# Optimization experiments

Hardware: AMD Instinct MI355X
Metric: run time of the kernel (lower is better)

The kernel has to match this reference:

```python
import jax, jax.numpy as jnp
import numpy as np

KDIM = 8192
EPS = 1e-8  # F.cosine_similarity default eps


def _encoder(x, W1, b1, W2, b2, W3, b3):
    # x: [..., KDIM] -> [..., 128]; Linear(KDIM,512)->ReLU->Linear(512,256)->ReLU->Linear(256,128)
    h = jax.nn.relu(x @ W1 + b1)
    h = jax.nn.relu(h @ W2 + b2)
    return h @ W3 + b3


def setup_inputs() -> dict:
    key = jax.random.key(0)
    ks = jax.random.split(key, 16)

    def lin(k, fan_in, fan_out):
        bound = 1.0 / np.sqrt(fan_in)
        kw, kb = jax.random.split(k)
        W = jax.random.uniform(kw, (fan_in, fan_out), jnp.float32, -bound, bound)
        b = jax.random.uniform(kb, (fan_out,), jnp.float32, -bound, bound)
        return W, b

    W1, b1 = lin(ks[0], KDIM, 512)
    W2, b2 = lin(ks[1], 512, 256)
    W3, b3 = lin(ks[2], 256, 128)
    Wi1, bi1 = lin(ks[3], 128 + 6, 64)
    Wi2, bi2 = lin(ks[4], 64, 32)
    Wi3, bi3 = lin(ks[5], 32, 1)

    return {
        "new_knowledge": jax.random.normal(ks[6], (KDIM,), jnp.float32),
        "existing_knowledge": jax.random.normal(ks[7], (10, KDIM), jnp.float32),
        "math_metrics": jax.random.uniform(ks[8], (6,), jnp.float32),
        "W1": W1, "b1": b1, "W2": W2, "b2": b2, "W3": W3, "b3": b3,
        "Wi1": Wi1, "bi1": bi1, "Wi2": Wi2, "bi2": bi2, "Wi3": Wi3, "bi3": bi3,
    }


def reference(new_knowledge, existing_knowledge, math_metrics,
              W1, b1, W2, b2, W3, b3, Wi1, bi1, Wi2, bi2, Wi3, bi3):
    # Encode new knowledge: [128]
    new_enc = _encoder(new_knowledge, W1, b1, W2, b2, W3, b3)
    # Batched encode of the (up to 10) existing knowledge vectors: [10, 128]
    ex_enc = _encoder(existing_knowledge, W1, b1, W2, b2, W3, b3)

    # Per-item geometric distance (L2 norm of difference)
    diff = new_enc[None, :] - ex_enc                     # [10, 128]
    geo_dist = jnp.sqrt(jnp.sum(diff * diff, axis=-1))   # [10]

    # Per-item cosine similarity with torch eps clamping
    new_n = jnp.maximum(jnp.linalg.norm(new_enc), EPS)
    ex_n = jnp.maximum(jnp.linalg.norm(ex_enc, axis=-1), EPS)  # [10]
    cos = (ex_enc @ new_enc) / (new_n * ex_n)            # [10]

    avg_consistency = jnp.mean(geo_dist - cos)

    # Mathematical-constraint integrator MLP on [128 + 6]
    combined = jnp.concatenate([new_enc, math_metrics])  # [134]
    h = jax.nn.relu(combined @ Wi1 + bi1)
    h = jax.nn.relu(h @ Wi2 + bi2)
    quality = h @ Wi3 + bi3                              # [1]

    integration_loss = jnp.exp(-quality)                 # [1]
    total = jnp.squeeze(avg_consistency + integration_loss)
    return total
```

## Files before the change

### kernel.cpp

```cpp
#include <hip/hip_runtime.h>
#include <math.h>

#define EPS 1e-8f
typedef float f32x4 __attribute__((ext_vector_type(4)));

__device__ __forceinline__ float wredsum(float v) {
#pragma unroll
  for (int o = 32; o > 0; o >>= 1) v += __shfl_down(v, o, 64);
  return v;
}

__device__ __forceinline__ void fma8(const float4* w, const float4 a,
                                     const float4 b, float4& c) {
  const float xs[8] = {a.x, a.y, a.z, a.w, b.x, b.y, b.z, b.w};
#pragma unroll
  for (int i = 0; i < 8; ++i) {
    c.x = fmaf(xs[i], w[i].x, c.x);
    c.y = fmaf(xs[i], w[i].y, c.y);
    c.z = fmaf(xs[i], w[i].z, c.z);
    c.w = fmaf(xs[i], w[i].w, c.w);
  }
}

__global__ __launch_bounds__(256, 2) void k_l1(const float* __restrict__ xn,
                                               const float* __restrict__ xe,
                                               const float* __restrict__ W1,
                                               float* __restrict__ p1,
                                               int* __restrict__ bars) {
  if (blockIdx.x == 0 && blockIdx.y == 0 && threadIdx.x == 0) {
    bars[0] = 0; bars[1] = 0;
  }
  __shared__ float red[11 * 32 * 36];
  const int cg  = threadIdx.x & 7;
  const int ks  = threadIdx.x >> 3;
  const int col = blockIdx.x * 32 + cg * 4;
  const int k0  = blockIdx.y * 256 + ks * 8;

  float4 w[8];
#pragma unroll
  for (int i = 0; i < 8; ++i)
    w[i] = *(const float4*)&W1[(size_t)(k0 + i) * 512 + col];

  float4 acc[11];
#pragma unroll
  for (int r = 0; r < 11; ++r) acc[r] = make_float4(0.f, 0.f, 0.f, 0.f);

  {
    const float4 a = *(const float4*)&xn[k0];
    const float4 b = *(const float4*)&xn[k0 + 4];
    fma8(w, a, b, acc[0]);
  }
#pragma unroll
  for (int r = 0; r < 10; ++r) {
    const float4 a = *(const float4*)&xe[r * 8192 + k0];
    const float4 b = *(const float4*)&xe[r * 8192 + k0 + 4];
    fma8(w, a, b, acc[r + 1]);
  }

#pragma unroll
  for (int r = 0; r < 11; ++r)
    *(float4*)&red[(r * 32 + ks) * 36 + cg * 4] = acc[r];
  __syncthreads();

  for (int o = threadIdx.x; o < 352; o += 256) {
    const int r = o >> 5, c = o & 31;
    float s = 0.f;
#pragma unroll
    for (int k = 0; k < 32; ++k) s += red[(r * 32 + k) * 36 + c];
    p1[((size_t)blockIdx.y * 11 + r) * 512 + blockIdx.x * 32 + c] = s;
  }
}

__global__ __launch_bounds__(1024) void k_tail(
    const float* __restrict__ p1, const float* __restrict__ b1,
    const float* __restrict__ W2, const float* __restrict__ b2,
    const float* __restrict__ W3, const float* __restrict__ b3,
    const float* __restrict__ mm,
    const float* __restrict__ Wi1, const float* __restrict__ bi1,
    const float* __restrict__ Wi2, const float* __restrict__ bi2,
    const float* __restrict__ Wi3, const float* __restrict__ bi3,
    float* __restrict__ p2, float* __restrict__ encp,
    int* __restrict__ bars, float* __restrict__ out) {
  __shared__ __align__(16) float smem[12368];
  __shared__ int tick;
  const int t = threadIdx.x;
  const int j = blockIdx.x;

  const int c = t & 255, kg = t >> 8;
  float w2r[8];
#pragma unroll
  for (int kk = 0; kk < 8; ++kk)
    w2r[kk] = W2[(size_t)(j * 32 + kg * 8 + kk) * 256 + c];

  float* h1s = smem;
  if (t < 352) {
    const int r = t >> 5, cc = t & 31;
    const int col = j * 32 + cc;
    float s = b1[col];
#pragma unroll
    for (int ch = 0; ch < 32; ++ch) s += p1[(size_t)(ch * 11 + r) * 512 + col];
    h1s[r * 32 + cc] = fmaxf(s, 0.f);
  }
  __syncthreads();

  float* redA = smem + 1024;
  {
    float acc[11];
#pragma unroll
    for (int r = 0; r < 11; ++r) acc[r] = 0.f;
#pragma unroll
    for (int kk = 0; kk < 8; ++kk) {
      const int kl = kg * 8 + kk;
#pragma unroll
      for (int r = 0; r < 11; ++r)
        acc[r] = fmaf(h1s[r * 32 + kl], w2r[kk], acc[r]);
    }
#pragma unroll
    for (int r = 0; r < 11; ++r) redA[(kg * 11 + r) * 256 + c] = acc[r];
  }
  __syncthreads();
  for (int o = t; o < 2816; o += 1024) {
    const int r = o >> 8, cc = o & 255;
    p2[(size_t)j * 2816 + o] = redA[r * 256 + cc] + redA[(11 + r) * 256 + cc] +
                               redA[(22 + r) * 256 + cc] +
                               redA[(33 + r) * 256 + cc];
  }

  __syncthreads();
  if (t == 0) {
    __threadfence();
    tick = __hip_atomic_fetch_add(&bars[0], 1, __ATOMIC_ACQ_REL,
                                  __HIP_MEMORY_SCOPE_AGENT);
  }
  __syncthreads();
  const int rank = tick;
  if (rank < 12) return;
  const int q = rank - 12;

  const int c3 = t & 127, kg3 = t >> 7;
  float w3r[8];
#pragma unroll
  for (int kk = 0; kk < 8; ++kk)
    w3r[kk] = W3[(size_t)(q * 64 + kg3 * 8 + kk) * 128 + c3];

  if (t == 0) {
    while (__hip_atomic_load(&bars[0], __ATOMIC_RELAXED,
                             __HIP_MEMORY_SCOPE_AGENT) < 16)
      __builtin_amdgcn_s_sleep(1);
    __threadfence();
  }
  __syncthreads();

  float* h2q = smem;
  if (t < 704) {
    const int r = t >> 6, kk = t & 63;
    const int col = q * 64 + kk;
    float s = b2[col];
#pragma unroll
    for (int jj = 0; jj < 16; ++jj) s += p2[(size_t)jj * 2816 + r * 256 + col];
    h2q[r * 64 + kk] = fmaxf(s, 0.f);
  }
  __syncthreads();
  float* redB = smem + 1024;
  {
    float acc[11];
#pragma unroll
    for (int r = 0; r < 11; ++r) acc[r] = 0.f;
#pragma unroll
    for (int kk = 0; kk < 8; ++kk) {
      const int kl = kg3 * 8 + kk;
#pragma unroll
      for (int r = 0; r < 11; ++r)
        acc[r] = fmaf(h2q[r * 64 + kl], w3r[kk], acc[r]);
    }
#pragma unroll
    for (int r = 0; r < 11; ++r) redB[(kg3 * 11 + r) * 128 + c3] = acc[r];
  }
  __syncthreads();
  for (int o = t; o < 1408; o += 1024) {
    const int r = o >> 7, cc = o & 127;
    float s = 0.f;
#pragma unroll
    for (int g = 0; g < 8; ++g) s += redB[(g * 11 + r) * 128 + cc];
    encp[(size_t)q * 1408 + o] = s;
  }

  __syncthreads();
  if (t == 0) {
    __threadfence();
    tick = __hip_atomic_fetch_add(&bars[1], 1, __ATOMIC_ACQ_REL,
                                  __HIP_MEMORY_SCOPE_AGENT);
  }
  __syncthreads();
  if (tick != 3) return;
  if (t == 0) __threadfence();
  __syncthreads();

  float* encs = smem;
  float* wi1s = smem + 1536;
  float* wi2s = smem + 10112;
  float* comb = smem + 12160;
  float* h1b  = smem + 12296;
  for (int i = t; i < 2144; i += 1024)
    ((f32x4*)wi1s)[i] = ((const f32x4*)Wi1)[i];
  if (t < 512) ((f32x4*)wi2s)[t] = ((const f32x4*)Wi2)[t];
  for (int o = t; o < 1408; o += 1024) {
    float s = b3[o & 127];
#pragma unroll
    for (int g = 0; g < 4; ++g) s += encp[(size_t)g * 1408 + o];
    encs[o] = s;
  }
  __syncthreads();

  float consist = 0.f;
  float n0 = 0.f, n1 = 0.f;
  if (t < 64) {
    n0 = encs[t]; n1 = encs[64 + t];
    comb[t] = n0; comb[64 + t] = n1;
    if (t < 6) comb[128 + t] = mm[t];
  }
  __syncthreads();
  if (t < 64) {
    const float nn = wredsum(n0 * n0 + n1 * n1);
#pragma unroll
    for (int r = 1; r <= 10; ++r) {
      const float e0 = encs[r * 128 + t];
      const float e1 = encs[r * 128 + 64 + t];
      const float d0 = e0 - n0, d1 = e1 - n1;
      const float g  = wredsum(d0 * d0 + d1 * d1);
      const float qq = wredsum(e0 * e0 + e1 * e1);
      const float dd = wredsum(e0 * n0 + e1 * n1);
      if (t == 0) {
        const float geo = sqrtf(g);
        const float den = fmaxf(sqrtf(nn), EPS) * fmaxf(sqrtf(qq), EPS);
        consist += geo - dd / den;
      }
    }
  } else if (t < 128) {
    const int tt = t - 64;
    float h = bi1[tt];
#pragma unroll 4
    for (int k = 0; k < 134; ++k) h = fmaf(comb[k], wi1s[k * 64 + tt], h);
    h1b[tt] = fmaxf(h, 0.f);
  }
  __syncthreads();
  if (t < 64) {
    float part = 0.f;
    if (t < 32) {
      float hh = bi2[t];
#pragma unroll 8
      for (int k = 0; k < 64; ++k) hh = fmaf(h1b[k], wi2s[k * 32 + t], hh);
      part = fmaxf(hh, 0.f) * Wi3[t];
    }
    const float qual = wredsum(part);
    if (t == 0) out[0] = consist * 0.1f + expf(-(qual + bi3[0]));
  }
}

extern "C" void kernel_launch(void* const* d_in, const int* in_sizes, int n_in,
                              void* d_out, int out_size, void* d_ws, size_t ws_size,
                              hipStream_t stream) {
  (void)in_sizes; (void)n_in; (void)out_size; (void)ws_size;
  const float* xn  = (const float*)d_in[0];
  const float* xe  = (const float*)d_in[1];
  const float* mm  = (const float*)d_in[2];
  const float* W1  = (const float*)d_in[3];
  const float* b1  = (const float*)d_in[4];
  const float* W2  = (const float*)d_in[5];
  const float* b2  = (const float*)d_in[6];
  const float* W3  = (const float*)d_in[7];
  const float* b3  = (const float*)d_in[8];
  const float* Wi1 = (const float*)d_in[9];
  const float* bi1 = (const float*)d_in[10];
  const float* Wi2 = (const float*)d_in[11];
  const float* bi2 = (const float*)d_in[12];
  const float* Wi3 = (const float*)d_in[13];
  const float* bi3 = (const float*)d_in[14];
  float* out = (float*)d_out;

  char* ws = (char*)d_ws;
  float* p1   = (float*)(ws);
  float* p2   = (float*)(ws + 720896);
  float* encp = (float*)(ws + 901120);
  int*   bars = (int*)  (ws + 923648);

  hipLaunchKernelGGL(k_l1,   dim3(16, 32), dim3(256),  0, stream, xn, xe, W1, p1, bars);
  hipLaunchKernelGGL(k_tail, dim3(16),     dim3(1024), 0, stream,
                     p1, b1, W2, b2, W3, b3, mm,
                     Wi1, bi1, Wi2, bi2, Wi3, bi3, p2, encp, bars, out);
}
```

Baseline: 109.4 us.

## Fuse layer-1 and tail kernels into one launch with per-tile flag dependencies

```diff
diff --git a/kernel.cpp b/kernel.cpp
--- a/kernel.cpp
+++ b/kernel.cpp
@@ -2,12 +2,19 @@
 #include <math.h>
 
 #define EPS 1e-8f
+#define MAGIC 0x1F2E3D4C
 typedef float f32x4 __attribute__((ext_vector_type(4)));
 
 __device__ __forceinline__ float wredsum(float v) {
 #pragma unroll
   for (int o = 32; o > 0; o >>= 1) v += __shfl_down(v, o, 64);
   return v;
+}
+
+__device__ __forceinline__ void waitflag(const int* f) {
+  while (__hip_atomic_load(f, __ATOMIC_RELAXED, __HIP_MEMORY_SCOPE_AGENT) !=
+         MAGIC)
+    __builtin_amdgcn_s_sleep(2);
 }
 
 __device__ __forceinline__ void fma8(const float4* w, const float4 a,
@@ -22,79 +29,86 @@
   }
 }
 
-__global__ __launch_bounds__(256, 2) void k_l1(const float* __restrict__ xn,
-                                               const float* __restrict__ xe,
-                                               const float* __restrict__ W1,
-                                               float* __restrict__ p1,
-                                               int* __restrict__ bars) {
-  if (blockIdx.x == 0 && blockIdx.y == 0 && threadIdx.x == 0) {
-    bars[0] = 0; bars[1] = 0;
-  }
-  __shared__ float red[11 * 32 * 36];
-  const int cg  = threadIdx.x & 7;
-  const int ks  = threadIdx.x >> 3;
-  const int col = blockIdx.x * 32 + cg * 4;
-  const int k0  = blockIdx.y * 256 + ks * 8;
-
-  float4 w[8];
-#pragma unroll
-  for (int i = 0; i < 8; ++i)
-    w[i] = *(const float4*)&W1[(size_t)(k0 + i) * 512 + col];
-
-  float4 acc[11];
-#pragma unroll
-  for (int r = 0; r < 11; ++r) acc[r] = make_float4(0.f, 0.f, 0.f, 0.f);
-
-  {
-    const float4 a = *(const float4*)&xn[k0];
-    const float4 b = *(const float4*)&xn[k0 + 4];
-    fma8(w, a, b, acc[0]);
-  }
-#pragma unroll
-  for (int r = 0; r < 10; ++r) {
-    const float4 a = *(const float4*)&xe[r * 8192 + k0];
-    const float4 b = *(const float4*)&xe[r * 8192 + k0 + 4];
-    fma8(w, a, b, acc[r + 1]);
-  }
-
-#pragma unroll
-  for (int r = 0; r < 11; ++r)
-    *(float4*)&red[(r * 32 + ks) * 36 + cg * 4] = acc[r];
-  __syncthreads();
-
-  for (int o = threadIdx.x; o < 352; o += 256) {
-    const int r = o >> 5, c = o & 31;
-    float s = 0.f;
-#pragma unroll
-    for (int k = 0; k < 32; ++k) s += red[(r * 32 + k) * 36 + c];
-    p1[((size_t)blockIdx.y * 11 + r) * 512 + blockIdx.x * 32 + c] = s;
-  }
-}
-
-__global__ __launch_bounds__(1024) void k_tail(
-    const float* __restrict__ p1, const float* __restrict__ b1,
+__global__ __launch_bounds__(256, 2) void k_all(
+    const float* __restrict__ xn, const float* __restrict__ xe,
+    const float* __restrict__ W1, const float* __restrict__ b1,
     const float* __restrict__ W2, const float* __restrict__ b2,
     const float* __restrict__ W3, const float* __restrict__ b3,
     const float* __restrict__ mm,
     const float* __restrict__ Wi1, const float* __restrict__ bi1,
     const float* __restrict__ Wi2, const float* __restrict__ bi2,
     const float* __restrict__ Wi3, const float* __restrict__ bi3,
-    float* __restrict__ p2, float* __restrict__ encp,
-    int* __restrict__ bars, float* __restrict__ out) {
-  __shared__ __align__(16) float smem[12368];
-  __shared__ int tick;
+    float* __restrict__ p1, float* __restrict__ p2, float* __restrict__ encp,
+    int* __restrict__ fA, int* __restrict__ fB, int* __restrict__ fC,
+    float* __restrict__ out) {
+  __shared__ __align__(16) float smem[12672];
   const int t = threadIdx.x;
-  const int j = blockIdx.x;
-
-  const int c = t & 255, kg = t >> 8;
-  float w2r[8];
-#pragma unroll
-  for (int kk = 0; kk < 8; ++kk)
-    w2r[kk] = W2[(size_t)(j * 32 + kg * 8 + kk) * 256 + c];
+  const int b = blockIdx.x;
+
+  if (b < 512) {
+    const int bx = b & 15, by = b >> 4;
+    const int cg = t & 7, ks = t >> 3;
+    const int col = bx * 32 + cg * 4;
+    const int k0  = by * 256 + ks * 8;
+
+    float4 w[8];
+#pragma unroll
+    for (int i = 0; i < 8; ++i)
+      w[i] = *(const float4*)&W1[(size_t)(k0 + i) * 512 + col];
+
+    float4 acc[11];
+#pragma unroll
+    for (int r = 0; r < 11; ++r) acc[r] = make_float4(0.f, 0.f, 0.f, 0.f);
+    {
+      const float4 a = *(const float4*)&xn[k0];
+      const float4 bb = *(const float4*)&xn[k0 + 4];
+      fma8(w, a, bb, acc[0]);
+    }
+#pragma unroll
+    for (int r = 0; r < 10; ++r) {
+      const float4 a = *(const float4*)&xe[r * 8192 + k0];
+      const float4 bb = *(const float4*)&xe[r * 8192 + k0 + 4];
+      fma8(w, a, bb, acc[r + 1]);
+    }
+
+    float* red = smem;
+#pragma unroll
+    for (int r = 0; r < 11; ++r)
+      *(float4*)&red[(r * 32 + ks) * 36 + cg * 4] = acc[r];
+    __syncthreads();
+
+    for (int o = t; o < 352; o += 256) {
+      const int r = o >> 5, c = o & 31;
+      float s = 0.f;
+#pragma unroll
+      for (int k = 0; k < 32; ++k) s += red[(r * 32 + k) * 36 + c];
+      p1[((size_t)by * 11 + r) * 512 + bx * 32 + c] = s;
+    }
+    __syncthreads();
+    if (t == 0) {
+      __threadfence();
+      __hip_atomic_store(&fA[b], MAGIC, __ATOMIC_RELAXED,
+                         __HIP_MEMORY_SCOPE_AGENT);
+    }
+    return;
+  }
+
+  const int j = b - 512;
+  const int c = t;
+
+  float w2r[32];
+#pragma unroll
+  for (int i = 0; i < 32; ++i)
+    w2r[i] = W2[(size_t)(j * 32 + i) * 256 + c];
+
+  if (t < 32) waitflag(&fA[j + 16 * t]);
+  __syncthreads();
+  if (t == 0) __threadfence();
+  __syncthreads();
 
   float* h1s = smem;
-  if (t < 352) {
-    const int r = t >> 5, cc = t & 31;
+  for (int o = t; o < 352; o += 256) {
+    const int r = o >> 5, cc = o & 31;
     const int col = j * 32 + cc;
     float s = b1[col];
 #pragma unroll
@@ -102,9 +116,9 @@
     h1s[r * 32 + cc] = fmaxf(s, 0.f);
   }
   __syncthreads();
-
   float* redA = smem + 1024;
-  {
+#pragma unroll
+  for (int kg = 0; kg < 4; ++kg) {
     float acc[11];
 #pragma unroll
     for (int r = 0; r < 11; ++r) acc[r] = 0.f;
@@ -113,47 +127,53 @@
       const int kl = kg * 8 + kk;
 #pragma unroll
       for (int r = 0; r < 11; ++r)
-        acc[r] = fmaf(h1s[r * 32 + kl], w2r[kk], acc[r]);
+        acc[r] = fmaf(h1s[r * 32 + kl], w2r[kg * 8 + kk], acc[r]);
     }
 #pragma unroll
     for (int r = 0; r < 11; ++r) redA[(kg * 11 + r) * 256 + c] = acc[r];
   }
   __syncthreads();
-  for (int o = t; o < 2816; o += 1024) {
+  for (int o = t; o < 2816; o += 256) {
     const int r = o >> 8, cc = o & 255;
     p2[(size_t)j * 2816 + o] = redA[r * 256 + cc] + redA[(11 + r) * 256 + cc] +
                                redA[(22 + r) * 256 + cc] +
                                redA[(33 + r) * 256 + cc];
   }
-
   __syncthreads();
   if (t == 0) {
     __threadfence();
-    tick = __hip_atomic_fetch_add(&bars[0], 1, __ATOMIC_ACQ_REL,
-                                  __HIP_MEMORY_SCOPE_AGENT);
-  }
-  __syncthreads();
-  const int rank = tick;
-  if (rank < 12) return;
-  const int q = rank - 12;
-
-  const int c3 = t & 127, kg3 = t >> 7;
-  float w3r[8];
-#pragma unroll
-  for (int kk = 0; kk < 8; ++kk)
-    w3r[kk] = W3[(size_t)(q * 64 + kg3 * 8 + kk) * 128 + c3];
-
-  if (t == 0) {
-    while (__hip_atomic_load(&bars[0], __ATOMIC_RELAXED,
-                             __HIP_MEMORY_SCOPE_AGENT) < 16)
-      __builtin_amdgcn_s_sleep(1);
-    __threadfence();
-  }
+    __hip_atomic_store(&fB[j], MAGIC, __ATOMIC_RELAXED,
+                       __HIP_MEMORY_SCOPE_AGENT);
+  }
+
+  if (j < 12) {
+    float dead = 0.f;
+    const int g = j * 256 + t;
+    if (g < 2144)      dead += ((const f32x4*)Wi1)[g][0];
+    else if (g < 2656) dead += ((const f32x4*)Wi2)[g - 2144][0];
+    else if (g < 2672) dead += ((const f32x4*)bi1)[g - 2656][0];
+    else if (g < 2704) dead += ((const f32x4*)b3)[g - 2672][0];
+    else if (g < 2712) dead += ((const f32x4*)bi2)[g - 2704][0];
+    else if (g < 2720) dead += ((const f32x4*)Wi3)[g - 2712][0];
+    asm volatile("" ::"v"(dead));
+    return;
+  }
+  const int q = j - 12;
+
+  const int c3 = t & 127, half = t >> 7;
+  float w3r[32];
+#pragma unroll
+  for (int i = 0; i < 32; ++i)
+    w3r[i] = W3[(size_t)(q * 64 + half * 32 + i) * 128 + c3];
+
+  if (t < 16) waitflag(&fB[t]);
+  __syncthreads();
+  if (t == 0) __threadfence();
   __syncthreads();
 
   float* h2q = smem;
-  if (t < 704) {
-    const int r = t >> 6, kk = t & 63;
+  for (int o = t; o < 704; o += 256) {
+    const int r = o >> 6, kk = o & 63;
     const int col = q * 64 + kk;
     float s = b2[col];
 #pragma unroll
@@ -162,7 +182,9 @@
   }
   __syncthreads();
   float* redB = smem + 1024;
-  {
+#pragma unroll
+  for (int m = 0; m < 4; ++m) {
+    const int kg3 = half * 4 + m;
     float acc[11];
 #pragma unroll
     for (int r = 0; r < 11; ++r) acc[r] = 0.f;
@@ -171,28 +193,29 @@
       const int kl = kg3 * 8 + kk;
 #pragma unroll
       for (int r = 0; r < 11; ++r)
-        acc[r] = fmaf(h2q[r * 64 + kl], w3r[kk], acc[r]);
+        acc[r] = fmaf(h2q[r * 64 + kl], w3r[m * 8 + kk], acc[r]);
     }
 #pragma unroll
     for (int r = 0; r < 11; ++r) redB[(kg3 * 11 + r) * 128 + c3] = acc[r];
   }
   __syncthreads();
-  for (int o = t; o < 1408; o += 1024) {
+  for (int o = t; o < 1408; o += 256) {
     const int r = o >> 7, cc = o & 127;
     float s = 0.f;
 #pragma unroll
     for (int g = 0; g < 8; ++g) s += redB[(g * 11 + r) * 128 + cc];
     encp[(size_t)q * 1408 + o] = s;
   }
-
   __syncthreads();
   if (t == 0) {
     __threadfence();
-    tick = __hip_atomic_fetch_add(&bars[1], 1, __ATOMIC_ACQ_REL,
-                                  __HIP_MEMORY_SCOPE_AGENT);
-  }
-  __syncthreads();
-  if (tick != 3) return;
+    __hip_atomic_store(&fC[q], MAGIC, __ATOMIC_RELAXED,
+                       __HIP_MEMORY_SCOPE_AGENT);
+  }
+  if (j != 15) return;
+
+  if (t < 4) waitflag(&fC[t]);
+  __syncthreads();
   if (t == 0) __threadfence();
   __syncthreads();
 
@@ -201,10 +224,11 @@
   float* wi2s = smem + 10112;
   float* comb = smem + 12160;
   float* h1b  = smem + 12296;
-  for (int i = t; i < 2144; i += 1024)
+  for (int i = t; i < 2144; i += 256)
     ((f32x4*)wi1s)[i] = ((const f32x4*)Wi1)[i];
-  if (t < 512) ((f32x4*)wi2s)[t] = ((const f32x4*)Wi2)[t];
-  for (int o = t; o < 1408; o += 1024) {
+  for (int i = t; i < 512; i += 256)
+    ((f32x4*)wi2s)[i] = ((const f32x4*)Wi2)[i];
+  for (int o = t; o < 1408; o += 256) {
     float s = b3[o & 127];
 #pragma unroll
     for (int g = 0; g < 4; ++g) s += encp[(size_t)g * 1408 + o];
@@ -238,10 +262,10 @@
     }
   } else if (t < 128) {
     const int tt = t - 64;
-    float h = bi1[tt];
+    float hh = bi1[tt];
 #pragma unroll 4
-    for (int k = 0; k < 134; ++k) h = fmaf(comb[k], wi1s[k * 64 + tt], h);
-    h1b[tt] = fmaxf(h, 0.f);
+    for (int k = 0; k < 134; ++k) hh = fmaf(comb[k], wi1s[k * 64 + tt], hh);
+    h1b[tt] = fmaxf(hh, 0.f);
   }
   __syncthreads();
   if (t < 64) {
@@ -255,6 +279,14 @@
     const float qual = wredsum(part);
     if (t == 0) out[0] = consist * 0.1f + expf(-(qual + bi3[0]));
   }
+
+  __syncthreads();
+  for (int i = t; i < 512; i += 256)
+    __hip_atomic_store(&fA[i], 0, __ATOMIC_RELAXED, __HIP_MEMORY_SCOPE_AGENT);
+  if (t < 16)
+    __hip_atomic_store(&fB[t], 0, __ATOMIC_RELAXED, __HIP_MEMORY_SCOPE_AGENT);
+  if (t < 4)
+    __hip_atomic_store(&fC[t], 0, __ATOMIC_RELAXED, __HIP_MEMORY_SCOPE_AGENT);
 }
 
 extern "C" void kernel_launch(void* const* d_in, const int* in_sizes, int n_in,
@@ -282,10 +314,12 @@
   float* p1   = (float*)(ws);
   float* p2   = (float*)(ws + 720896);
   float* encp = (float*)(ws + 901120);
-  int*   bars = (int*)  (ws + 923648);
-
-  hipLaunchKernelGGL(k_l1,   dim3(16, 32), dim3(256),  0, stream, xn, xe, W1, p1, bars);
-  hipLaunchKernelGGL(k_tail, dim3(16),     dim3(1024), 0, stream,
-                     p1, b1, W2, b2, W3, b3, mm,
-                     Wi1, bi1, Wi2, bi2, Wi3, bi3, p2, encp, bars, out);
-}
+  int*   fA   = (int*)  (ws + 923648);
+  int*   fB   = (int*)  (ws + 925696);
+  int*   fC   = (int*)  (ws + 925760);
+
+  hipLaunchKernelGGL(k_all, dim3(528), dim3(256), 0, stream,
+                     xn, xe, W1, b1, W2, b2, W3, b3, mm,
+                     Wi1, bi1, Wi2, bi2, Wi3, bi3,
+                     p1, p2, encp, fA, fB, fC, out);
+}
```

Measured after the change: 127.7 us. 1.17x slower.

## Split tail kernel into role-specialized blocks with per-block ready flags

Applied to the files above, without the earlier changes.

```diff
diff --git a/kernel.cpp b/kernel.cpp
--- a/kernel.cpp
+++ b/kernel.cpp
@@ -2,12 +2,19 @@
 #include <math.h>
 
 #define EPS 1e-8f
+#define MAGIC 0x1F2E3D4C
 typedef float f32x4 __attribute__((ext_vector_type(4)));
 
 __device__ __forceinline__ float wredsum(float v) {
 #pragma unroll
   for (int o = 32; o > 0; o >>= 1) v += __shfl_down(v, o, 64);
   return v;
+}
+
+__device__ __forceinline__ void waitflag(const int* f) {
+  while (__hip_atomic_load(f, __ATOMIC_RELAXED, __HIP_MEMORY_SCOPE_AGENT) !=
+         MAGIC)
+    __builtin_amdgcn_s_sleep(2);
 }
 
 __device__ __forceinline__ void fma8(const float4* w, const float4 a,
@@ -26,10 +33,9 @@
                                                const float* __restrict__ xe,
                                                const float* __restrict__ W1,
                                                float* __restrict__ p1,
-                                               int* __restrict__ bars) {
-  if (blockIdx.x == 0 && blockIdx.y == 0 && threadIdx.x == 0) {
-    bars[0] = 0; bars[1] = 0;
-  }
+                                               int* __restrict__ flg) {
+  if (blockIdx.x == 0 && blockIdx.y == 0 && threadIdx.x < 40)
+    flg[threadIdx.x] = 0;
   __shared__ float red[11 * 32 * 36];
   const int cg  = threadIdx.x & 7;
   const int ks  = threadIdx.x >> 3;
@@ -44,7 +50,6 @@
   float4 acc[11];
 #pragma unroll
   for (int r = 0; r < 11; ++r) acc[r] = make_float4(0.f, 0.f, 0.f, 0.f);
-
   {
     const float4 a = *(const float4*)&xn[k0];
     const float4 b = *(const float4*)&xn[k0 + 4];
@@ -71,7 +76,7 @@
   }
 }
 
-__global__ __launch_bounds__(1024) void k_tail(
+__global__ __launch_bounds__(256) void k_tail(
     const float* __restrict__ p1, const float* __restrict__ b1,
     const float* __restrict__ W2, const float* __restrict__ b2,
     const float* __restrict__ W3, const float* __restrict__ b3,
@@ -80,134 +85,123 @@
     const float* __restrict__ Wi2, const float* __restrict__ bi2,
     const float* __restrict__ Wi3, const float* __restrict__ bi3,
     float* __restrict__ p2, float* __restrict__ encp,
-    int* __restrict__ bars, float* __restrict__ out) {
-  __shared__ __align__(16) float smem[12368];
-  __shared__ int tick;
+    int* __restrict__ flg, float* __restrict__ out) {
+  __shared__ __align__(16) float smem[12672];
   const int t = threadIdx.x;
   const int j = blockIdx.x;
 
-  const int c = t & 255, kg = t >> 8;
-  float w2r[8];
-#pragma unroll
-  for (int kk = 0; kk < 8; ++kk)
-    w2r[kk] = W2[(size_t)(j * 32 + kg * 8 + kk) * 256 + c];
-
-  float* h1s = smem;
-  if (t < 352) {
-    const int r = t >> 5, cc = t & 31;
-    const int col = j * 32 + cc;
-    float s = b1[col];
-#pragma unroll
-    for (int ch = 0; ch < 32; ++ch) s += p1[(size_t)(ch * 11 + r) * 512 + col];
-    h1s[r * 32 + cc] = fmaxf(s, 0.f);
-  }
-  __syncthreads();
-
-  float* redA = smem + 1024;
-  {
+  if (j < 32) {
+    float w2r[16];
+#pragma unroll
+    for (int i = 0; i < 16; ++i)
+      w2r[i] = W2[(size_t)(j * 16 + i) * 256 + t];
+
+    float* h1s = smem;
+    if (t < 176) {
+      const int r = t >> 4, cc = t & 15;
+      const int col = j * 16 + cc;
+      float s = b1[col];
+#pragma unroll
+      for (int ch = 0; ch < 32; ++ch)
+        s += p1[(size_t)(ch * 11 + r) * 512 + col];
+      h1s[r * 16 + cc] = fmaxf(s, 0.f);
+    }
+    __syncthreads();
+
     float acc[11];
 #pragma unroll
     for (int r = 0; r < 11; ++r) acc[r] = 0.f;
 #pragma unroll
-    for (int kk = 0; kk < 8; ++kk) {
-      const int kl = kg * 8 + kk;
+    for (int kk = 0; kk < 16; ++kk) {
 #pragma unroll
       for (int r = 0; r < 11; ++r)
-        acc[r] = fmaf(h1s[r * 32 + kl], w2r[kk], acc[r]);
-    }
-#pragma unroll
-    for (int r = 0; r < 11; ++r) redA[(kg * 11 + r) * 256 + c] = acc[r];
-  }
-  __syncthreads();
-  for (int o = t; o < 2816; o += 1024) {
-    const int r = o >> 8, cc = o & 255;
-    p2[(size_t)j * 2816 + o] = redA[r * 256 + cc] + redA[(11 + r) * 256 + cc] +
-                               redA[(22 + r) * 256 + cc] +
-                               redA[(33 + r) * 256 + cc];
-  }
-
-  __syncthreads();
-  if (t == 0) {
-    __threadfence();
-    tick = __hip_atomic_fetch_add(&bars[0], 1, __ATOMIC_ACQ_REL,
-                                  __HIP_MEMORY_SCOPE_AGENT);
-  }
-  __syncthreads();
-  const int rank = tick;
-  if (rank < 12) return;
-  const int q = rank - 12;
-
-  const int c3 = t & 127, kg3 = t >> 7;
-  float w3r[8];
-#pragma unroll
-  for (int kk = 0; kk < 8; ++kk)
-    w3r[kk] = W3[(size_t)(q * 64 + kg3 * 8 + kk) * 128 + c3];
-
-  if (t == 0) {
-    while (__hip_atomic_load(&bars[0], __ATOMIC_RELAXED,
-                             __HIP_MEMORY_SCOPE_AGENT) < 16)
-      __builtin_amdgcn_s_sleep(1);
-    __threadfence();
-  }
-  __syncthreads();
-
-  float* h2q = smem;
-  if (t < 704) {
-    const int r = t >> 6, kk = t & 63;
-    const int col = q * 64 + kk;
-    float s = b2[col];
-#pragma unroll
-    for (int jj = 0; jj < 16; ++jj) s += p2[(size_t)jj * 2816 + r * 256 + col];
-    h2q[r * 64 + kk] = fmaxf(s, 0.f);
-  }
-  __syncthreads();
-  float* redB = smem + 1024;
-  {
-    float acc[11];
-#pragma unroll
-    for (int r = 0; r < 11; ++r) acc[r] = 0.f;
-#pragma unroll
-    for (int kk = 0; kk < 8; ++kk) {
-      const int kl = kg3 * 8 + kk;
-#pragma unroll
-      for (int r = 0; r < 11; ++r)
-        acc[r] = fmaf(h2q[r * 64 + kl], w3r[kk], acc[r]);
-    }
-#pragma unroll
-    for (int r = 0; r < 11; ++r) redB[(kg3 * 11 + r) * 128 + c3] = acc[r];
-  }
-  __syncthreads();
-  for (int o = t; o < 1408; o += 1024) {
-    const int r = o >> 7, cc = o & 127;
-    float s = 0.f;
-#pragma unroll
-    for (int g = 0; g < 8; ++g) s += redB[(g * 11 + r) * 128 + cc];
-    encp[(size_t)q * 1408 + o] = s;
-  }
-
-  __syncthreads();
-  if (t == 0) {
-    __threadfence();
-    tick = __hip_atomic_fetch_add(&bars[1], 1, __ATOMIC_ACQ_REL,
-                                  __HIP_MEMORY_SCOPE_AGENT);
-  }
-  __syncthreads();
-  if (tick != 3) return;
-  if (t == 0) __threadfence();
-  __syncthreads();
+        acc[r] = fmaf(h1s[r * 16 + kk], w2r[kk], acc[r]);
+    }
+    const int q = t >> 5, cc = t & 31;
+#pragma unroll
+    for (int r = 0; r < 11; ++r)
+      p2[((size_t)q * 32 + j) * 352 + r * 32 + cc] = acc[r];
+
+    __syncthreads();
+    if (t == 0) {
+      __threadfence();
+      __hip_atomic_store(&flg[j], MAGIC, __ATOMIC_RELAXED,
+                         __HIP_MEMORY_SCOPE_AGENT);
+    }
+    return;
+  }
+
+  if (j < 40) {
+    const int q = j - 32;
+    const int c3 = t & 127, half = t >> 7;
+    float w3r[16];
+#pragma unroll
+    for (int i = 0; i < 16; ++i)
+      w3r[i] = W3[(size_t)(q * 32 + half * 16 + i) * 128 + c3];
+
+    if (t < 32) waitflag(&flg[t]);
+    __syncthreads();
+    if (t == 0) __threadfence();
+    __syncthreads();
+
+    float* h2q = smem;
+    for (int o = t; o < 352; o += 256) {
+      const int r = o >> 5, kk = o & 31;
+      float s = b2[q * 32 + kk];
+#pragma unroll
+      for (int jj = 0; jj < 32; ++jj)
+        s += p2[((size_t)q * 32 + jj) * 352 + r * 32 + kk];
+      h2q[r * 32 + kk] = fmaxf(s, 0.f);
+    }
+    __syncthreads();
+
+    float* redB = smem + 512;
+    {
+      float acc[11];
+#pragma unroll
+      for (int r = 0; r < 11; ++r) acc[r] = 0.f;
+#pragma unroll
+      for (int i = 0; i < 16; ++i) {
+        const int kk = half * 16 + i;
+#pragma unroll
+        for (int r = 0; r < 11; ++r)
+          acc[r] = fmaf(h2q[r * 32 + kk], w3r[i], acc[r]);
+      }
+#pragma unroll
+      for (int r = 0; r < 11; ++r) redB[(half * 11 + r) * 128 + c3] = acc[r];
+    }
+    __syncthreads();
+    for (int o = t; o < 1408; o += 256)
+      encp[(size_t)q * 1408 + o] = redB[o] + redB[1408 + o];
+
+    __syncthreads();
+    if (t == 0) {
+      __threadfence();
+      __hip_atomic_store(&flg[32 + q], MAGIC, __ATOMIC_RELAXED,
+                         __HIP_MEMORY_SCOPE_AGENT);
+    }
+    return;
+  }
 
   float* encs = smem;
   float* wi1s = smem + 1536;
   float* wi2s = smem + 10112;
   float* comb = smem + 12160;
   float* h1b  = smem + 12296;
-  for (int i = t; i < 2144; i += 1024)
+  for (int i = t; i < 2144; i += 256)
     ((f32x4*)wi1s)[i] = ((const f32x4*)Wi1)[i];
-  if (t < 512) ((f32x4*)wi2s)[t] = ((const f32x4*)Wi2)[t];
-  for (int o = t; o < 1408; o += 1024) {
+  for (int i = t; i < 512; i += 256)
+    ((f32x4*)wi2s)[i] = ((const f32x4*)Wi2)[i];
+
+  if (t < 8) waitflag(&flg[32 + t]);
+  __syncthreads();
+  if (t == 0) __threadfence();
+  __syncthreads();
+
+  for (int o = t; o < 1408; o += 256) {
     float s = b3[o & 127];
 #pragma unroll
-    for (int g = 0; g < 4; ++g) s += encp[(size_t)g * 1408 + o];
+    for (int g = 0; g < 8; ++g) s += encp[(size_t)g * 1408 + o];
     encs[o] = s;
   }
   __syncthreads();
@@ -238,10 +232,10 @@
     }
   } else if (t < 128) {
     const int tt = t - 64;
-    float h = bi1[tt];
+    float hh = bi1[tt];
 #pragma unroll 4
-    for (int k = 0; k < 134; ++k) h = fmaf(comb[k], wi1s[k * 64 + tt], h);
-    h1b[tt] = fmaxf(h, 0.f);
+    for (int k = 0; k < 134; ++k) hh = fmaf(comb[k], wi1s[k * 64 + tt], hh);
+    h1b[tt] = fmaxf(hh, 0.f);
   }
   __syncthreads();
   if (t < 64) {
@@ -281,11 +275,12 @@
   char* ws = (char*)d_ws;
   float* p1   = (float*)(ws);
   float* p2   = (float*)(ws + 720896);
-  float* encp = (float*)(ws + 901120);
-  int*   bars = (int*)  (ws + 923648);
-
-  hipLaunchKernelGGL(k_l1,   dim3(16, 32), dim3(256),  0, stream, xn, xe, W1, p1, bars);
-  hipLaunchKernelGGL(k_tail, dim3(16),     dim3(1024), 0, stream,
+  float* encp = (float*)(ws + 1081344);
+  int*   flg  = (int*)  (ws + 1126400);
+
+  hipLaunchKernelGGL(k_l1,   dim3(16, 32), dim3(256), 0, stream,
+                     xn, xe, W1, p1, flg);
+  hipLaunchKernelGGL(k_tail, dim3(41),     dim3(256), 0, stream,
                      p1, b1, W2, b2, W3, b3, mm,
-                     Wi1, bi1, Wi2, bi2, Wi3, bi3, p2, encp, bars, out);
-}
+                     Wi1, bi1, Wi2, bi2, Wi3, bi3, p2, encp, flg, out);
+}
```

Result: no change. 110.7 us (+1.1%).
